# Kernel optimization log

Hardware: AMD Instinct MI355X
Metric: run time of the kernel (lower is better)

The kernel has to match this reference:

```python
import jax, jax.numpy as jnp
import numpy as np


def _unfold(x, k, stride, pad):
    """torch.nn.Unfold equivalent. x: [B,C,H,W] -> [B, C*k*k, L] with
    channel ordering (c, ki, kj) slow->fast and L = oh*ow row-major."""
    if pad:
        x = jnp.pad(x, ((0, 0), (0, 0), (pad, pad), (pad, pad)))
    B, C, H, W = x.shape
    oh = (H - k) // stride + 1
    ow = (W - k) // stride + 1
    r = jnp.arange(oh) * stride
    c = jnp.arange(ow) * stride
    xr = x[:, :, r[:, None] + jnp.arange(k)[None, :], :]          # [B,C,oh,k,W]
    xc = xr[:, :, :, :, c[:, None] + jnp.arange(k)[None, :]]      # [B,C,oh,ki,ow,kj]
    p = xc.transpose(0, 1, 3, 5, 2, 4)                            # [B,C,ki,kj,oh,ow]
    return p.reshape(B, C * k * k, oh * ow)


def _resize_bilinear(x, h, w):
    # matches F.interpolate(mode='bilinear', align_corners=False) for upsampling
    B, C = x.shape[0], x.shape[1]
    return jax.image.resize(x, (B, C, h, w), method='bilinear')


def setup_inputs() -> dict:
    key = jax.random.key(0)
    ks = jax.random.split(key, 8)
    bs, C, NC = 16, 768, 200
    x = jax.random.normal(ks[0], (bs, 784, C), jnp.float32)
    mask = jax.random.uniform(ks[1], (bs, 81), dtype=jnp.float32)
    img = jax.random.normal(ks[2], (bs, 3, 448, 448), jnp.float32)
    W_fc = jax.random.normal(ks[3], (NC, C), jnp.float32) * 0.02
    b_fc = jnp.zeros((NC,), jnp.float32)
    W_l = jax.random.normal(ks[4], (192, C), jnp.float32) * 0.02
    b_l = jnp.zeros((192,), jnp.float32)
    W_m = jax.random.normal(ks[5], (192, C), jnp.float32) * 0.02
    b_m = jnp.zeros((192,), jnp.float32)
    W_s = jax.random.normal(ks[6], (384, C), jnp.float32) * 0.02
    b_s = jnp.zeros((384,), jnp.float32)
    return dict(x=x, mask=mask, img=img, W_fc=W_fc, b_fc=b_fc,
                W_l=W_l, b_l=b_l, W_m=W_m, b_m=b_m, W_s=W_s, b_s=b_s)


def reference(x, mask, img, W_fc, b_fc, W_l, b_l, W_m, b_m, W_s, b_s):
    bs, C = x.shape[0], 768
    # im2col over image and feature map (all produce 81 = 9x9 windows)
    image_patches = _unfold(img, 128, 48, 32).transpose(0, 2, 1)   # [bs,81,3*128*128]
    feat = x.transpose(0, 2, 1).reshape(bs, C, 28, 28)
    patches_l = _unfold(feat, 8, 3, 2).transpose(0, 2, 1)          # [bs,81,C*64]
    patches_m = _unfold(feat, 6, 3, 1).transpose(0, 2, 1)          # [bs,81,C*36]
    patches_s = _unfold(feat, 4, 3, 0).transpose(0, 2, 1)          # [bs,81,C*16]
    # per-token class probabilities -> per-window importance score
    prob = jax.nn.softmax(x @ W_fc.T + b_fc, axis=-1)              # [bs,784,NC]
    max_logits = prob.max(axis=-1).reshape(bs, 1, 28, 28)
    part_logits = _unfold(max_logits, 8, 3, 2).mean(axis=1)        # [bs,81]
    part_logits = mask * part_logits
    sel = jnp.argmax(part_logits, axis=-1)                         # top-1 window id
    b_idx = jnp.arange(bs)
    parts_l = patches_l[b_idx, sel]                                # [bs,C*64]
    parts_m = patches_m[b_idx, sel]                                # [bs,C*36]
    parts_s = patches_s[b_idx, sel]                                # [bs,C*16]
    image_parts = image_patches[b_idx, sel]                        # [bs,3*128*128]
    # fold (single patch => reshape) + bilinear upsample to 8x8
    outl = parts_l.reshape(bs, C, 8, 8).transpose(0, 2, 3, 1).reshape(bs, 64, C)
    outm = _resize_bilinear(parts_m.reshape(bs, C, 6, 6), 8, 8)
    outm = outm.transpose(0, 2, 3, 1).reshape(bs, 64, C)
    outs = _resize_bilinear(parts_s.reshape(bs, C, 4, 4), 8, 8)
    outs = outs.transpose(0, 2, 3, 1).reshape(bs, 64, C)
    part1 = outl @ W_l.T + b_l                                     # [bs,64,192]
    part2 = outm @ W_m.T + b_m                                     # [bs,64,192]
    part3 = outs @ W_s.T + b_s                                     # [bs,64,384]
    ff_cat = jnp.concatenate([part1, part2, part3], axis=2)        # [bs,64,768]
    image_part = _resize_bilinear(image_parts.reshape(bs, 3, 128, 128), 224, 224)
    return ff_cat, image_part
```

## Files before the change

kernel.cpp:

```cpp
#include <hip/hip_runtime.h>
#include <math.h>

typedef __attribute__((ext_vector_type(8))) short bf16x8;
typedef __attribute__((ext_vector_type(4))) float f32x4;

__device__ __forceinline__ unsigned short f32_to_bf16_rne(float f) {
    unsigned int u = __float_as_uint(f);
    unsigned int r = (u + 0x7FFFu + ((u >> 16) & 1u)) >> 16;
    return (unsigned short)r;
}
__device__ __forceinline__ float bf16_to_f32(unsigned short h) {
    return __uint_as_float(((unsigned int)h) << 16);
}
__device__ __forceinline__ unsigned int pck(unsigned short a, unsigned short b) {
    return (unsigned int)a | ((unsigned int)b << 16);
}

__global__ __launch_bounds__(256) void k_split(
    const float* __restrict__ src, unsigned short* __restrict__ hi,
    unsigned short* __restrict__ lo, int src_rows, int nq)
{
    const int idx = blockIdx.x * 256 + threadIdx.x;
    if (idx >= nq) return;
    const int c = idx / 192;
    const int kk = (idx % 192) * 4;
    unsigned short h[4] = {0, 0, 0, 0}, l[4] = {0, 0, 0, 0};
    if (c < src_rows) {
        const float4 w = *(const float4*)&src[(size_t)c * 768 + kk];
        const float wv[4] = {w.x, w.y, w.z, w.w};
#pragma unroll
        for (int j = 0; j < 4; ++j) {
            h[j] = f32_to_bf16_rne(wv[j]);
            l[j] = f32_to_bf16_rne(wv[j] - bf16_to_f32(h[j]));
        }
    }
    *(uint2*)&hi[(size_t)c * 768 + kk] = make_uint2(pck(h[0], h[1]), pck(h[2], h[3]));
    *(uint2*)&lo[(size_t)c * 768 + kk] = make_uint2(pck(l[0], l[1]), pck(l[2], l[3]));
}

__global__ __launch_bounds__(256) void k_logits(
    const float* __restrict__ x, const unsigned short* __restrict__ Whi,
    const unsigned short* __restrict__ Wlo, float* __restrict__ logits)
{
    __shared__ unsigned short Ah[4][64][8], Alo[4][64][8];
    __shared__ unsigned short Bh[8][64][8], Blo[8][64][8];
    const int tid = threadIdx.x;
    const int lane = tid & 63;
    const int wid = tid >> 6;
    const int wm = wid & 1, wn = wid >> 1;
    const int row0 = blockIdx.x * 64;
    const int n0 = blockIdx.y * 128;

    f32x4 acc[2][4];
    const f32x4 z = {0.f, 0.f, 0.f, 0.f};
#pragma unroll
    for (int mi = 0; mi < 2; ++mi)
#pragma unroll
        for (int q = 0; q < 4; ++q) acc[mi][q] = z;

    const int ar = tid & 63;
    const int ap = tid >> 6;
    const int bc = tid >> 1;
    const int bkh = tid & 1;

    for (int kc = 0; kc < 768; kc += 32) {
        __syncthreads();
        {
            const float* src = &x[(size_t)(row0 + ar) * 768 + kc + ap * 8];
            const float4 v0 = *(const float4*)src;
            const float4 v1 = *(const float4*)(src + 4);
            const float av[8] = {v0.x, v0.y, v0.z, v0.w, v1.x, v1.y, v1.z, v1.w};
            unsigned short h[8], l[8];
#pragma unroll
            for (int j = 0; j < 8; ++j) {
                h[j] = f32_to_bf16_rne(av[j]);
                l[j] = f32_to_bf16_rne(av[j] - bf16_to_f32(h[j]));
            }
            const int m = ar >> 4, ci = ar & 15;
            *(uint4*)&Ah[m][ap * 16 + ci][0] =
                make_uint4(pck(h[0], h[1]), pck(h[2], h[3]), pck(h[4], h[5]), pck(h[6], h[7]));
            *(uint4*)&Alo[m][ap * 16 + ci][0] =
                make_uint4(pck(l[0], l[1]), pck(l[2], l[3]), pck(l[4], l[5]), pck(l[6], l[7]));
        }
        {
            const size_t off = (size_t)(n0 + bc) * 768 + kc + bkh * 16;
            const uint4 h0 = *(const uint4*)&Whi[off];
            const uint4 h1 = *(const uint4*)&Whi[off + 8];
            const uint4 l0 = *(const uint4*)&Wlo[off];
            const uint4 l1 = *(const uint4*)&Wlo[off + 8];
            const int q = bc >> 4, ci = bc & 15;
            *(uint4*)&Bh[q][(2 * bkh) * 16 + ci][0] = h0;
            *(uint4*)&Bh[q][(2 * bkh + 1) * 16 + ci][0] = h1;
            *(uint4*)&Blo[q][(2 * bkh) * 16 + ci][0] = l0;
            *(uint4*)&Blo[q][(2 * bkh + 1) * 16 + ci][0] = l1;
        }
        __syncthreads();

        bf16x8 a_h[2], a_l[2];
#pragma unroll
        for (int mi = 0; mi < 2; ++mi) {
            a_h[mi] = *(const bf16x8*)&Ah[wm * 2 + mi][lane][0];
            a_l[mi] = *(const bf16x8*)&Alo[wm * 2 + mi][lane][0];
        }
#pragma unroll
        for (int q = 0; q < 4; ++q) {
            const bf16x8 bh = *(const bf16x8*)&Bh[wn * 4 + q][lane][0];
            const bf16x8 bl = *(const bf16x8*)&Blo[wn * 4 + q][lane][0];
#pragma unroll
            for (int mi = 0; mi < 2; ++mi) {
                acc[mi][q] = __builtin_amdgcn_mfma_f32_16x16x32_bf16(a_l[mi], bh, acc[mi][q], 0, 0, 0);
                acc[mi][q] = __builtin_amdgcn_mfma_f32_16x16x32_bf16(a_h[mi], bl, acc[mi][q], 0, 0, 0);
                acc[mi][q] = __builtin_amdgcn_mfma_f32_16x16x32_bf16(a_h[mi], bh, acc[mi][q], 0, 0, 0);
            }
        }
    }

#pragma unroll
    for (int mi = 0; mi < 2; ++mi)
#pragma unroll
        for (int q = 0; q < 4; ++q)
#pragma unroll
            for (int r = 0; r < 4; ++r) {
                const int row = row0 + wm * 32 + mi * 16 + (lane >> 4) * 4 + r;
                const int col = n0 + wn * 64 + q * 16 + (lane & 15);
                logits[(size_t)row * 256 + col] = acc[mi][q][r];
            }
}

__global__ __launch_bounds__(256) void k_softmax(
    const float* __restrict__ logits, const float* __restrict__ bfc,
    float* __restrict__ maxprob)
{
    const int row = blockIdx.x * 4 + (threadIdx.x >> 6);
    const int lane = threadIdx.x & 63;
    float v[4];
    float m = -1e30f;
#pragma unroll
    for (int j = 0; j < 4; ++j) {
        const int c = lane + j * 64;
        v[j] = (c < 200) ? (logits[(size_t)row * 256 + c] + bfc[c]) : -1e30f;
        m = fmaxf(m, v[j]);
    }
#pragma unroll
    for (int s = 32; s; s >>= 1) m = fmaxf(m, __shfl_xor(m, s, 64));
    float se = 0.f;
#pragma unroll
    for (int j = 0; j < 4; ++j) {
        const int c = lane + j * 64;
        if (c < 200) se += __expf(v[j] - m);
    }
#pragma unroll
    for (int s = 32; s; s >>= 1) se += __shfl_xor(se, s, 64);
    if (lane == 0) maxprob[row] = 1.0f / se;
}

__global__ void k_sel(const float* __restrict__ maxprob,
                      const float* __restrict__ mask, int* __restrict__ sel)
{
    __shared__ float mp[784];
    __shared__ float pl[81];
    const int b = blockIdx.x, tid = threadIdx.x;
    for (int i = tid; i < 784; i += blockDim.x) mp[i] = maxprob[b * 784 + i];
    __syncthreads();
    if (tid < 81) {
        const int pr = tid / 9, pc = tid % 9;
        float s = 0.f;
        for (int ki = 0; ki < 8; ++ki) {
            const int y = pr * 3 - 2 + ki;
            if (y < 0 || y >= 28) continue;
            for (int kj = 0; kj < 8; ++kj) {
                const int xx = pc * 3 - 2 + kj;
                if (xx < 0 || xx >= 28) continue;
                s += mp[y * 28 + xx];
            }
        }
        pl[tid] = mask[b * 81 + tid] * (s * (1.f / 64.f));
    }
    __syncthreads();
    if (tid == 0) {
        float best = pl[0]; int bi = 0;
        for (int i = 1; i < 81; ++i) if (pl[i] > best) { best = pl[i]; bi = i; }
        sel[b] = bi;
    }
}

__device__ __forceinline__ void rcoef8(int o, int n, int& f0, int& f1, float& w)
{
    float s = (o + 0.5f) * ((float)n * 0.125f) - 0.5f;
    s = fminf(fmaxf(s, 0.f), (float)(n - 1));
    f0 = (int)s;
    w = s - (float)f0;
    f1 = f0 + 1; if (f1 > n - 1) f1 = n - 1;
}

__global__ __launch_bounds__(256) void k_ff(
    const float* __restrict__ x, const int* __restrict__ sel,
    const unsigned short* __restrict__ Whi2, const unsigned short* __restrict__ Wlo2,
    const float* __restrict__ bl, const float* __restrict__ bm,
    const float* __restrict__ bs_, float* __restrict__ out)
{
    __shared__ float W8[64][33];
    __shared__ unsigned short Ah[4][64][8], Alo[4][64][8];
    __shared__ unsigned short Bh[4][64][8], Blo[4][64][8];

    const int blk = blockIdx.x;
    const int b = blk / 12, t = blk % 12;
    const int n0 = t * 64;
    const int seg = (t < 3) ? 0 : ((t < 6) ? 1 : 2);
    const float* bias = (seg == 0) ? (bl + t * 64)
                      : (seg == 1) ? (bm + (t - 3) * 64)
                                   : (bs_ + (t - 6) * 64);
    const int s = sel[b];
    const int wy0 = (s / 9) * 3 - 2, wx0 = (s % 9) * 3 - 2;

    const int tid = threadIdx.x;
    const int lane = tid & 63;
    const int wid = tid >> 6, wmi = wid & 1, wn = wid >> 1;

    const int gp = tid & 63;
    const int gy = wy0 + (gp >> 3), gx = wx0 + (gp & 7);
    const bool inb = (gy >= 0 && gy < 28 && gx >= 0 && gx < 28);
    const float* xsrc = x + ((size_t)b * 784 + (inb ? (gy * 28 + gx) : 0)) * 768;
    const int ko = (tid >> 6) * 8;

    const int ai = tid & 63;
    int r00, r01, r10, r11; float fx = 0.f, fy = 0.f;
    if (seg == 0) { r00 = r01 = r10 = r11 = ai; }
    else {
        const int nn = (seg == 1) ? 6 : 4, off = (seg == 1) ? 1 : 2;
        int f0y, f1y, f0x, f1x;
        rcoef8(ai >> 3, nn, f0y, f1y, fy);
        rcoef8(ai & 7, nn, f0x, f1x, fx);
        r00 = (off + f0y) * 8 + off + f0x;
        r01 = (off + f0y) * 8 + off + f1x;
        r10 = (off + f1y) * 8 + off + f0x;
        r11 = (off + f1y) * 8 + off + f1x;
    }

    const int bc = tid >> 2, kq = tid & 3;
    const unsigned short* WhP = Whi2 + (size_t)(n0 + bc) * 768 + kq * 8;
    const unsigned short* WlP = Wlo2 + (size_t)(n0 + bc) * 768 + kq * 8;

    f32x4 acc[2][2];
    const f32x4 z = {0.f, 0.f, 0.f, 0.f};
#pragma unroll
    for (int mi = 0; mi < 2; ++mi)
#pragma unroll
        for (int q = 0; q < 2; ++q) acc[mi][q] = z;

    for (int kc = 0; kc < 768; kc += 32) {
        __syncthreads();
        {
            float v[8] = {0, 0, 0, 0, 0, 0, 0, 0};
            if (inb) {
                const float4 a0 = *(const float4*)(xsrc + kc + ko);
                const float4 a1 = *(const float4*)(xsrc + kc + ko + 4);
                v[0] = a0.x; v[1] = a0.y; v[2] = a0.z; v[3] = a0.w;
                v[4] = a1.x; v[5] = a1.y; v[6] = a1.z; v[7] = a1.w;
            }
#pragma unroll
            for (int j = 0; j < 8; ++j) W8[gp][ko + j] = v[j];
        }
        {
            const uint4 h = *(const uint4*)(WhP + kc);
            const uint4 l = *(const uint4*)(WlP + kc);
            *(uint4*)&Bh[bc >> 4][kq * 16 + (bc & 15)][0] = h;
            *(uint4*)&Blo[bc >> 4][kq * 16 + (bc & 15)][0] = l;
        }
        __syncthreads();
        {
            unsigned short h[8], l[8];
#pragma unroll
            for (int j = 0; j < 8; ++j) {
                const int k = ko + j;
                const float g00 = W8[r00][k], g01 = W8[r01][k];
                const float g10 = W8[r10][k], g11 = W8[r11][k];
                const float v0 = g00 + fx * (g01 - g00);
                const float v1 = g10 + fx * (g11 - g10);
                const float a = v0 + fy * (v1 - v0);
                h[j] = f32_to_bf16_rne(a);
                l[j] = f32_to_bf16_rne(a - bf16_to_f32(h[j]));
            }
            const int m = ai >> 4, ci = ai & 15, p2 = ko >> 3;
            *(uint4*)&Ah[m][p2 * 16 + ci][0] =
                make_uint4(pck(h[0], h[1]), pck(h[2], h[3]), pck(h[4], h[5]), pck(h[6], h[7]));
            *(uint4*)&Alo[m][p2 * 16 + ci][0] =
                make_uint4(pck(l[0], l[1]), pck(l[2], l[3]), pck(l[4], l[5]), pck(l[6], l[7]));
        }
        __syncthreads();

        bf16x8 a_h[2], a_l[2];
#pragma unroll
        for (int mi = 0; mi < 2; ++mi) {
            a_h[mi] = *(const bf16x8*)&Ah[wmi * 2 + mi][lane][0];
            a_l[mi] = *(const bf16x8*)&Alo[wmi * 2 + mi][lane][0];
        }
#pragma unroll
        for (int q = 0; q < 2; ++q) {
            const bf16x8 bh = *(const bf16x8*)&Bh[wn * 2 + q][lane][0];
            const bf16x8 bl2 = *(const bf16x8*)&Blo[wn * 2 + q][lane][0];
#pragma unroll
            for (int mi = 0; mi < 2; ++mi) {
                acc[mi][q] = __builtin_amdgcn_mfma_f32_16x16x32_bf16(a_l[mi], bh, acc[mi][q], 0, 0, 0);
                acc[mi][q] = __builtin_amdgcn_mfma_f32_16x16x32_bf16(a_h[mi], bl2, acc[mi][q], 0, 0, 0);
                acc[mi][q] = __builtin_amdgcn_mfma_f32_16x16x32_bf16(a_h[mi], bh, acc[mi][q], 0, 0, 0);
            }
        }
    }

#pragma unroll
    for (int mi = 0; mi < 2; ++mi)
#pragma unroll
        for (int q = 0; q < 2; ++q)
#pragma unroll
            for (int r = 0; r < 4; ++r) {
                const int row = wmi * 32 + mi * 16 + (lane >> 4) * 4 + r;
                const int col = wn * 32 + q * 16 + (lane & 15);
                out[((size_t)b * 64 + row) * 768 + n0 + col] = acc[mi][q][r] + bias[col];
            }
}

__global__ __launch_bounds__(256) void k_image(
    const float* __restrict__ img, const int* __restrict__ sel,
    float* __restrict__ out)
{
    const int idx = blockIdx.x * 256 + threadIdx.x;
    if (idx >= 16 * 3 * 224 * 224) return;
    const int ox = idx % 224;
    int t = idx / 224;
    const int oy = t % 224; t /= 224;
    const int c = t % 3;
    const int b = t / 3;
    const int s = sel[b];
    const int ry0 = (s / 9) * 48 - 32, cx0 = (s % 9) * 48 - 32;

    float sy = (oy + 0.5f) * (128.f / 224.f) - 0.5f;
    sy = fminf(fmaxf(sy, 0.f), 127.f);
    const int fy0 = (int)sy; const float wy = sy - (float)fy0;
    const int fy1 = (fy0 < 127) ? fy0 + 1 : 127;

    float sx = (ox + 0.5f) * (128.f / 224.f) - 0.5f;
    sx = fminf(fmaxf(sx, 0.f), 127.f);
    const int fx0 = (int)sx; const float wx = sx - (float)fx0;
    const int fx1 = (fx0 < 127) ? fx0 + 1 : 127;

    const float* ib = img + ((size_t)b * 3 + c) * 448 * 448;
    auto rd = [&](int py, int px) -> float {
        const int r = ry0 + py, cc = cx0 + px;
        return (r >= 0 && r < 448 && cc >= 0 && cc < 448) ? ib[r * 448 + cc] : 0.f;
    };
    const float g00 = rd(fy0, fx0), g01 = rd(fy0, fx1);
    const float g10 = rd(fy1, fx0), g11 = rd(fy1, fx1);
    const float v0 = g00 + wx * (g01 - g00);
    const float v1 = g10 + wx * (g11 - g10);
    out[idx] = v0 + wy * (v1 - v0);
}

extern "C" void kernel_launch(void* const* d_in, const int* in_sizes, int n_in,
                              void* d_out, int out_size, void* d_ws, size_t ws_size,
                              hipStream_t stream)
{
    const float* x    = (const float*)d_in[0];
    const float* mask = (const float*)d_in[1];
    const float* img  = (const float*)d_in[2];
    const float* Wfc  = (const float*)d_in[3];
    const float* bfc  = (const float*)d_in[4];
    const float* Wl   = (const float*)d_in[5];
    const float* bl   = (const float*)d_in[6];
    const float* Wm   = (const float*)d_in[7];
    const float* bm   = (const float*)d_in[8];
    const float* Ws   = (const float*)d_in[9];
    const float* bs   = (const float*)d_in[10];
    float* out = (float*)d_out;

    char* ws = (char*)d_ws;
    float* maxprob      = (float*)ws;
    int*   sel          = (int*)(ws + 51200);
    unsigned short* Whi  = (unsigned short*)(ws + 65536);
    unsigned short* Wlo  = (unsigned short*)(ws + 65536 + 393216);
    unsigned short* Whi2 = (unsigned short*)(ws + 917504);
    unsigned short* Wlo2 = (unsigned short*)(ws + 917504 + 1179648);
    float* logits = (float*)(ws + 3276800);

    hipLaunchKernelGGL(k_split, dim3(192), dim3(256), 0, stream, Wfc, Whi, Wlo, 200, 256 * 192);
    hipLaunchKernelGGL(k_split, dim3(144), dim3(256), 0, stream, Wl, Whi2, Wlo2, 192, 192 * 192);
    hipLaunchKernelGGL(k_split, dim3(144), dim3(256), 0, stream,
                       Wm, Whi2 + (size_t)192 * 768, Wlo2 + (size_t)192 * 768, 192, 192 * 192);
    hipLaunchKernelGGL(k_split, dim3(288), dim3(256), 0, stream,
                       Ws, Whi2 + (size_t)384 * 768, Wlo2 + (size_t)384 * 768, 384, 384 * 192);

    hipLaunchKernelGGL(k_logits,  dim3(196, 2), dim3(256), 0, stream, x, Whi, Wlo, logits);
    hipLaunchKernelGGL(k_softmax, dim3(3136),   dim3(256), 0, stream, logits, bfc, maxprob);
    hipLaunchKernelGGL(k_sel,     dim3(16),     dim3(128), 0, stream, maxprob, mask, sel);
    hipLaunchKernelGGL(k_ff,      dim3(192),    dim3(256), 0, stream,
                       x, sel, Whi2, Wlo2, bl, bm, bs, out);
    hipLaunchKernelGGL(k_image,   dim3(9408),   dim3(256), 0, stream,
                       img, sel, out + 786432);
}
```

Measured before the change: 215.9 us.

## Fuse logits GEMM with softmax, pre-pack weights, double-buffer GEMM loops

The four weight-split launches are merged into one prep kernel. It writes bf16 hi/lo weights directly in the MFMA-ready LDS tile layout, so the GEMM kernels can copy them with coalesced uint4 loads. The logits GEMM now covers all 256 columns per block and computes the softmax max-probability in its epilogue, which removes the logits buffer round trip and the separate softmax kernel. Both GEMMs use register-prefetched double-buffered LDS with one barrier per k-step, and k_ff does the bilinear gather with wave shuffles instead of an fp32 LDS staging tile. The costs are higher register and LDS use per block and only 196 blocks for the logits GEMM.

```diff
diff --git a/kernel.cpp b/kernel.cpp
--- a/kernel.cpp
+++ b/kernel.cpp
@@ -16,16 +16,22 @@
     return (unsigned int)a | ((unsigned int)b << 16);
 }
 
-__global__ __launch_bounds__(256) void k_split(
-    const float* __restrict__ src, unsigned short* __restrict__ hi,
-    unsigned short* __restrict__ lo, int src_rows, int nq)
-{
-    const int idx = blockIdx.x * 256 + threadIdx.x;
-    if (idx >= nq) return;
+__global__ __launch_bounds__(256) void k_prep(
+    const float* __restrict__ Wfc, const float* __restrict__ Wl,
+    const float* __restrict__ Wm, const float* __restrict__ Ws,
+    unsigned short* __restrict__ Bpkh, unsigned short* __restrict__ Bpkl,
+    unsigned short* __restrict__ B2h, unsigned short* __restrict__ B2l)
+{
+    const int blk = blockIdx.x, tid = threadIdx.x;
+    const float* src; int idx, rows, cbase; bool isfc;
+    if (blk < 192)      { isfc = true;  idx = blk * 256 + tid;        src = Wfc; rows = 200; cbase = 0; }
+    else if (blk < 336) { isfc = false; idx = (blk - 192) * 256 + tid; src = Wl;  rows = 192; cbase = 0; }
+    else if (blk < 480) { isfc = false; idx = (blk - 336) * 256 + tid; src = Wm;  rows = 192; cbase = 192; }
+    else                { isfc = false; idx = (blk - 480) * 256 + tid; src = Ws;  rows = 384; cbase = 384; }
     const int c = idx / 192;
     const int kk = (idx % 192) * 4;
     unsigned short h[4] = {0, 0, 0, 0}, l[4] = {0, 0, 0, 0};
-    if (c < src_rows) {
+    if (c < rows) {
         const float4 w = *(const float4*)&src[(size_t)c * 768 + kk];
         const float wv[4] = {w.x, w.y, w.z, w.w};
 #pragma unroll
@@ -34,124 +40,160 @@
             l[j] = f32_to_bf16_rne(wv[j] - bf16_to_f32(h[j]));
         }
     }
-    *(uint2*)&hi[(size_t)c * 768 + kk] = make_uint2(pck(h[0], h[1]), pck(h[2], h[3]));
-    *(uint2*)&lo[(size_t)c * 768 + kk] = make_uint2(pck(l[0], l[1]), pck(l[2], l[3]));
-}
-
-__global__ __launch_bounds__(256) void k_logits(
-    const float* __restrict__ x, const unsigned short* __restrict__ Whi,
-    const unsigned short* __restrict__ Wlo, float* __restrict__ logits)
-{
-    __shared__ unsigned short Ah[4][64][8], Alo[4][64][8];
-    __shared__ unsigned short Bh[8][64][8], Blo[8][64][8];
+    const int step = kk >> 5, oct = (kk & 31) >> 3, elem = kk & 7;
+    const uint2 uh = make_uint2(pck(h[0], h[1]), pck(h[2], h[3]));
+    const uint2 ul = make_uint2(pck(l[0], l[1]), pck(l[2], l[3]));
+    if (isfc) {
+        const size_t off = (size_t)((step * 16 + (c >> 4)) * 64 + oct * 16 + (c & 15)) * 8 + elem;
+        *(uint2*)&Bpkh[off] = uh;
+        *(uint2*)&Bpkl[off] = ul;
+    } else {
+        const int cg = cbase + c;
+        const int tt = cg >> 6, cc = cg & 63;
+        const size_t off = (size_t)(((tt * 24 + step) * 4 + (cc >> 4)) * 64 + oct * 16 + (cc & 15)) * 8 + elem;
+        *(uint2*)&B2h[off] = uh;
+        *(uint2*)&B2l[off] = ul;
+    }
+}
+
+__global__ __launch_bounds__(256) void k_logits_fused(
+    const float* __restrict__ x, const unsigned short* __restrict__ Bpkh,
+    const unsigned short* __restrict__ Bpkl, const float* __restrict__ bfc,
+    float* __restrict__ maxprob)
+{
+    __shared__ unsigned short AhS[2][4][64][8];
+    __shared__ unsigned short AlS[2][4][64][8];
+    __shared__ unsigned short BhS[2][16][64][8];
+    __shared__ unsigned short BlS[2][16][64][8];
+    __shared__ float sbias[256];
+    __shared__ float red[4][64];
+    __shared__ float red2[4][64];
+
     const int tid = threadIdx.x;
     const int lane = tid & 63;
     const int wid = tid >> 6;
-    const int wm = wid & 1, wn = wid >> 1;
     const int row0 = blockIdx.x * 64;
-    const int n0 = blockIdx.y * 128;
-
-    f32x4 acc[2][4];
+
+    sbias[tid] = (tid < 200) ? bfc[tid] : -1e30f;
+
+    const int ar = tid & 63, ap = tid >> 6;
+    const float* xb = x + (size_t)(row0 + ar) * 768 + ap * 8;
+    const uint4* bhs = (const uint4*)Bpkh;
+    const uint4* bls = (const uint4*)Bpkl;
+
+    float ag[8];
+    uint4 bgh[4], bgl[4];
+
+    f32x4 acc[4][4];
     const f32x4 z = {0.f, 0.f, 0.f, 0.f};
 #pragma unroll
-    for (int mi = 0; mi < 2; ++mi)
-#pragma unroll
-        for (int q = 0; q < 4; ++q) acc[mi][q] = z;
-
-    const int ar = tid & 63;
-    const int ap = tid >> 6;
-    const int bc = tid >> 1;
-    const int bkh = tid & 1;
-
-    for (int kc = 0; kc < 768; kc += 32) {
+    for (int mf = 0; mf < 4; ++mf)
+#pragma unroll
+        for (int q = 0; q < 4; ++q) acc[mf][q] = z;
+
+    auto LOADAB = [&](int t) {
+        const float4 v0 = *(const float4*)(xb + t * 32);
+        const float4 v1 = *(const float4*)(xb + t * 32 + 4);
+        ag[0] = v0.x; ag[1] = v0.y; ag[2] = v0.z; ag[3] = v0.w;
+        ag[4] = v1.x; ag[5] = v1.y; ag[6] = v1.z; ag[7] = v1.w;
+#pragma unroll
+        for (int j = 0; j < 4; ++j) {
+            bgh[j] = bhs[t * 1024 + j * 256 + tid];
+            bgl[j] = bls[t * 1024 + j * 256 + tid];
+        }
+    };
+    auto WRITEAB = [&](int buf) {
+        unsigned short h[8], l[8];
+#pragma unroll
+        for (int j = 0; j < 8; ++j) {
+            h[j] = f32_to_bf16_rne(ag[j]);
+            l[j] = f32_to_bf16_rne(ag[j] - bf16_to_f32(h[j]));
+        }
+        *(uint4*)&AhS[buf][ar >> 4][ap * 16 + (ar & 15)][0] =
+            make_uint4(pck(h[0], h[1]), pck(h[2], h[3]), pck(h[4], h[5]), pck(h[6], h[7]));
+        *(uint4*)&AlS[buf][ar >> 4][ap * 16 + (ar & 15)][0] =
+            make_uint4(pck(l[0], l[1]), pck(l[2], l[3]), pck(l[4], l[5]), pck(l[6], l[7]));
+        uint4* bdh = (uint4*)&BhS[buf][0][0][0];
+        uint4* bdl = (uint4*)&BlS[buf][0][0][0];
+#pragma unroll
+        for (int j = 0; j < 4; ++j) {
+            bdh[j * 256 + tid] = bgh[j];
+            bdl[j * 256 + tid] = bgl[j];
+        }
+    };
+
+    LOADAB(0);
+    WRITEAB(0);
+    __syncthreads();
+
+    for (int t = 0; t < 24; ++t) {
+        const int cur = t & 1;
+        if (t < 23) LOADAB(t + 1);
+        bf16x8 ah[4], al2[4];
+#pragma unroll
+        for (int mf = 0; mf < 4; ++mf) {
+            ah[mf]  = *(const bf16x8*)&AhS[cur][mf][lane][0];
+            al2[mf] = *(const bf16x8*)&AlS[cur][mf][lane][0];
+        }
+#pragma unroll
+        for (int q = 0; q < 4; ++q) {
+            const bf16x8 bh = *(const bf16x8*)&BhS[cur][wid * 4 + q][lane][0];
+            const bf16x8 bl = *(const bf16x8*)&BlS[cur][wid * 4 + q][lane][0];
+#pragma unroll
+            for (int mf = 0; mf < 4; ++mf) {
+                acc[mf][q] = __builtin_amdgcn_mfma_f32_16x16x32_bf16(al2[mf], bh, acc[mf][q], 0, 0, 0);
+                acc[mf][q] = __builtin_amdgcn_mfma_f32_16x16x32_bf16(ah[mf], bl, acc[mf][q], 0, 0, 0);
+                acc[mf][q] = __builtin_amdgcn_mfma_f32_16x16x32_bf16(ah[mf], bh, acc[mf][q], 0, 0, 0);
+            }
+        }
+        if (t < 23) WRITEAB(cur ^ 1);
         __syncthreads();
-        {
-            const float* src = &x[(size_t)(row0 + ar) * 768 + kc + ap * 8];
-            const float4 v0 = *(const float4*)src;
-            const float4 v1 = *(const float4*)(src + 4);
-            const float av[8] = {v0.x, v0.y, v0.z, v0.w, v1.x, v1.y, v1.z, v1.w};
-            unsigned short h[8], l[8];
-#pragma unroll
-            for (int j = 0; j < 8; ++j) {
-                h[j] = f32_to_bf16_rne(av[j]);
-                l[j] = f32_to_bf16_rne(av[j] - bf16_to_f32(h[j]));
+    }
+
+    float bv[4];
+#pragma unroll
+    for (int q = 0; q < 4; ++q) bv[q] = sbias[wid * 64 + q * 16 + (lane & 15)];
+
+    float mrow[4][4];
+#pragma unroll
+    for (int mf = 0; mf < 4; ++mf)
+#pragma unroll
+        for (int r = 0; r < 4; ++r) {
+            float mx = -1e30f;
+#pragma unroll
+            for (int q = 0; q < 4; ++q) mx = fmaxf(mx, acc[mf][q][r] + bv[q]);
+#pragma unroll
+            for (int s = 1; s < 16; s <<= 1) mx = fmaxf(mx, __shfl_xor(mx, s, 64));
+            mrow[mf][r] = mx;
+            if ((lane & 15) == 0) red[wid][mf * 16 + (lane >> 4) * 4 + r] = mx;
+        }
+    __syncthreads();
+#pragma unroll
+    for (int mf = 0; mf < 4; ++mf)
+#pragma unroll
+        for (int r = 0; r < 4; ++r) {
+            const int row = mf * 16 + (lane >> 4) * 4 + r;
+            const float m = fmaxf(fmaxf(red[0][row], red[1][row]),
+                                  fmaxf(red[2][row], red[3][row]));
+            float se = 0.f;
+#pragma unroll
+            for (int q = 0; q < 4; ++q) se += __expf(acc[mf][q][r] + bv[q] - m);
+#pragma unroll
+            for (int s = 1; s < 16; s <<= 1) se += __shfl_xor(se, s, 64);
+            if ((lane & 15) == 0) red2[wid][row] = se;
+            (void)mrow[mf][r];
+        }
+    __syncthreads();
+    if (wid == 0 && (lane & 15) == 0) {
+#pragma unroll
+        for (int mf = 0; mf < 4; ++mf)
+#pragma unroll
+            for (int r = 0; r < 4; ++r) {
+                const int row = mf * 16 + (lane >> 4) * 4 + r;
+                maxprob[row0 + row] = 1.0f /
+                    (red2[0][row] + red2[1][row] + red2[2][row] + red2[3][row]);
             }
-            const int m = ar >> 4, ci = ar & 15;
-            *(uint4*)&Ah[m][ap * 16 + ci][0] =
-                make_uint4(pck(h[0], h[1]), pck(h[2], h[3]), pck(h[4], h[5]), pck(h[6], h[7]));
-            *(uint4*)&Alo[m][ap * 16 + ci][0] =
-                make_uint4(pck(l[0], l[1]), pck(l[2], l[3]), pck(l[4], l[5]), pck(l[6], l[7]));
-        }
-        {
-            const size_t off = (size_t)(n0 + bc) * 768 + kc + bkh * 16;
-            const uint4 h0 = *(const uint4*)&Whi[off];
-            const uint4 h1 = *(const uint4*)&Whi[off + 8];
-            const uint4 l0 = *(const uint4*)&Wlo[off];
-            const uint4 l1 = *(const uint4*)&Wlo[off + 8];
-            const int q = bc >> 4, ci = bc & 15;
-            *(uint4*)&Bh[q][(2 * bkh) * 16 + ci][0] = h0;
-            *(uint4*)&Bh[q][(2 * bkh + 1) * 16 + ci][0] = h1;
-            *(uint4*)&Blo[q][(2 * bkh) * 16 + ci][0] = l0;
-            *(uint4*)&Blo[q][(2 * bkh + 1) * 16 + ci][0] = l1;
-        }
-        __syncthreads();
-
-        bf16x8 a_h[2], a_l[2];
-#pragma unroll
-        for (int mi = 0; mi < 2; ++mi) {
-            a_h[mi] = *(const bf16x8*)&Ah[wm * 2 + mi][lane][0];
-            a_l[mi] = *(const bf16x8*)&Alo[wm * 2 + mi][lane][0];
-        }
-#pragma unroll
-        for (int q = 0; q < 4; ++q) {
-            const bf16x8 bh = *(const bf16x8*)&Bh[wn * 4 + q][lane][0];
-            const bf16x8 bl = *(const bf16x8*)&Blo[wn * 4 + q][lane][0];
-#pragma unroll
-            for (int mi = 0; mi < 2; ++mi) {
-                acc[mi][q] = __builtin_amdgcn_mfma_f32_16x16x32_bf16(a_l[mi], bh, acc[mi][q], 0, 0, 0);
-                acc[mi][q] = __builtin_amdgcn_mfma_f32_16x16x32_bf16(a_h[mi], bl, acc[mi][q], 0, 0, 0);
-                acc[mi][q] = __builtin_amdgcn_mfma_f32_16x16x32_bf16(a_h[mi], bh, acc[mi][q], 0, 0, 0);
-            }
-        }
-    }
-
-#pragma unroll
-    for (int mi = 0; mi < 2; ++mi)
-#pragma unroll
-        for (int q = 0; q < 4; ++q)
-#pragma unroll
-            for (int r = 0; r < 4; ++r) {
-                const int row = row0 + wm * 32 + mi * 16 + (lane >> 4) * 4 + r;
-                const int col = n0 + wn * 64 + q * 16 + (lane & 15);
-                logits[(size_t)row * 256 + col] = acc[mi][q][r];
-            }
-}
-
-__global__ __launch_bounds__(256) void k_softmax(
-    const float* __restrict__ logits, const float* __restrict__ bfc,
-    float* __restrict__ maxprob)
-{
-    const int row = blockIdx.x * 4 + (threadIdx.x >> 6);
-    const int lane = threadIdx.x & 63;
-    float v[4];
-    float m = -1e30f;
-#pragma unroll
-    for (int j = 0; j < 4; ++j) {
-        const int c = lane + j * 64;
-        v[j] = (c < 200) ? (logits[(size_t)row * 256 + c] + bfc[c]) : -1e30f;
-        m = fmaxf(m, v[j]);
-    }
-#pragma unroll
-    for (int s = 32; s; s >>= 1) m = fmaxf(m, __shfl_xor(m, s, 64));
-    float se = 0.f;
-#pragma unroll
-    for (int j = 0; j < 4; ++j) {
-        const int c = lane + j * 64;
-        if (c < 200) se += __expf(v[j] - m);
-    }
-#pragma unroll
-    for (int s = 32; s; s >>= 1) se += __shfl_xor(se, s, 64);
-    if (lane == 0) maxprob[row] = 1.0f / se;
+    }
 }
 
 __global__ void k_sel(const float* __restrict__ maxprob,
@@ -195,13 +237,14 @@
 
 __global__ __launch_bounds__(256) void k_ff(
     const float* __restrict__ x, const int* __restrict__ sel,
-    const unsigned short* __restrict__ Whi2, const unsigned short* __restrict__ Wlo2,
+    const unsigned short* __restrict__ B2h, const unsigned short* __restrict__ B2l,
     const float* __restrict__ bl, const float* __restrict__ bm,
     const float* __restrict__ bs_, float* __restrict__ out)
 {
-    __shared__ float W8[64][33];
-    __shared__ unsigned short Ah[4][64][8], Alo[4][64][8];
-    __shared__ unsigned short Bh[4][64][8], Blo[4][64][8];
+    __shared__ unsigned short AhS[2][4][64][8];
+    __shared__ unsigned short AlS[2][4][64][8];
+    __shared__ unsigned short BhS[2][4][64][8];
+    __shared__ unsigned short BlS[2][4][64][8];
 
     const int blk = blockIdx.x;
     const int b = blk / 12, t = blk % 12;
@@ -217,29 +260,28 @@
     const int lane = tid & 63;
     const int wid = tid >> 6, wmi = wid & 1, wn = wid >> 1;
 
-    const int gp = tid & 63;
-    const int gy = wy0 + (gp >> 3), gx = wx0 + (gp & 7);
+    const int gy = wy0 + (lane >> 3), gx = wx0 + (lane & 7);
     const bool inb = (gy >= 0 && gy < 28 && gx >= 0 && gx < 28);
-    const float* xsrc = x + ((size_t)b * 784 + (inb ? (gy * 28 + gx) : 0)) * 768;
-    const int ko = (tid >> 6) * 8;
-
-    const int ai = tid & 63;
+    const float* xsrc = x + ((size_t)b * 784 + (inb ? (gy * 28 + gx) : 0)) * 768 + wid * 8;
+
     int r00, r01, r10, r11; float fx = 0.f, fy = 0.f;
-    if (seg == 0) { r00 = r01 = r10 = r11 = ai; }
+    if (seg == 0) { r00 = r01 = r10 = r11 = lane; }
     else {
         const int nn = (seg == 1) ? 6 : 4, off = (seg == 1) ? 1 : 2;
         int f0y, f1y, f0x, f1x;
-        rcoef8(ai >> 3, nn, f0y, f1y, fy);
-        rcoef8(ai & 7, nn, f0x, f1x, fx);
+        rcoef8(lane >> 3, nn, f0y, f1y, fy);
+        rcoef8(lane & 7, nn, f0x, f1x, fx);
         r00 = (off + f0y) * 8 + off + f0x;
         r01 = (off + f0y) * 8 + off + f1x;
         r10 = (off + f1y) * 8 + off + f0x;
         r11 = (off + f1y) * 8 + off + f1x;
     }
 
-    const int bc = tid >> 2, kq = tid & 3;
-    const unsigned short* WhP = Whi2 + (size_t)(n0 + bc) * 768 + kq * 8;
-    const unsigned short* WlP = Wlo2 + (size_t)(n0 + bc) * 768 + kq * 8;
+    const uint4* b2h = (const uint4*)B2h + (size_t)t * 24 * 256;
+    const uint4* b2l = (const uint4*)B2l + (size_t)t * 24 * 256;
+
+    float g[8];
+    uint4 bh_r, bl_r;
 
     f32x4 acc[2][2];
     const f32x4 z = {0.f, 0.f, 0.f, 0.f};
@@ -248,64 +290,67 @@
 #pragma unroll
         for (int q = 0; q < 2; ++q) acc[mi][q] = z;
 
-    for (int kc = 0; kc < 768; kc += 32) {
+    auto LOAD = [&](int st) {
+        if (inb) {
+            const float4 v0 = *(const float4*)(xsrc + st * 32);
+            const float4 v1 = *(const float4*)(xsrc + st * 32 + 4);
+            g[0] = v0.x; g[1] = v0.y; g[2] = v0.z; g[3] = v0.w;
+            g[4] = v1.x; g[5] = v1.y; g[6] = v1.z; g[7] = v1.w;
+        } else {
+#pragma unroll
+            for (int j = 0; j < 8; ++j) g[j] = 0.f;
+        }
+        bh_r = b2h[st * 256 + tid];
+        bl_r = b2l[st * 256 + tid];
+    };
+    auto WRITE = [&](int buf) {
+        unsigned short h[8], l[8];
+#pragma unroll
+        for (int j = 0; j < 8; ++j) {
+            const float v00 = __shfl(g[j], r00, 64);
+            const float v01 = __shfl(g[j], r01, 64);
+            const float v10 = __shfl(g[j], r10, 64);
+            const float v11 = __shfl(g[j], r11, 64);
+            const float v0 = v00 + fx * (v01 - v00);
+            const float v1 = v10 + fx * (v11 - v10);
+            const float a = v0 + fy * (v1 - v0);
+            h[j] = f32_to_bf16_rne(a);
+            l[j] = f32_to_bf16_rne(a - bf16_to_f32(h[j]));
+        }
+        *(uint4*)&AhS[buf][lane >> 4][wid * 16 + (lane & 15)][0] =
+            make_uint4(pck(h[0], h[1]), pck(h[2], h[3]), pck(h[4], h[5]), pck(h[6], h[7]));
+        *(uint4*)&AlS[buf][lane >> 4][wid * 16 + (lane & 15)][0] =
+            make_uint4(pck(l[0], l[1]), pck(l[2], l[3]), pck(l[4], l[5]), pck(l[6], l[7]));
+        ((uint4*)&BhS[buf][0][0][0])[tid] = bh_r;
+        ((uint4*)&BlS[buf][0][0][0])[tid] = bl_r;
+    };
+
+    LOAD(0);
+    WRITE(0);
+    __syncthreads();
+
+    for (int st = 0; st < 24; ++st) {
+        const int cur = st & 1;
+        if (st < 23) LOAD(st + 1);
+        bf16x8 ah[2], al2[2];
+#pragma unroll
+        for (int mi = 0; mi < 2; ++mi) {
+            ah[mi]  = *(const bf16x8*)&AhS[cur][wmi * 2 + mi][lane][0];
+            al2[mi] = *(const bf16x8*)&AlS[cur][wmi * 2 + mi][lane][0];
+        }
+#pragma unroll
+        for (int q = 0; q < 2; ++q) {
+            const bf16x8 bh = *(const bf16x8*)&BhS[cur][wn * 2 + q][lane][0];
+            const bf16x8 bl2 = *(const bf16x8*)&BlS[cur][wn * 2 + q][lane][0];
+#pragma unroll
+            for (int mi = 0; mi < 2; ++mi) {
+                acc[mi][q] = __builtin_amdgcn_mfma_f32_16x16x32_bf16(al2[mi], bh, acc[mi][q], 0, 0, 0);
+                acc[mi][q] = __builtin_amdgcn_mfma_f32_16x16x32_bf16(ah[mi], bl2, acc[mi][q], 0, 0, 0);
+                acc[mi][q] = __builtin_amdgcn_mfma_f32_16x16x32_bf16(ah[mi], bh, acc[mi][q], 0, 0, 0);
+            }
+        }
+        if (st < 23) WRITE(cur ^ 1);
         __syncthreads();
-        {
-            float v[8] = {0, 0, 0, 0, 0, 0, 0, 0};
-            if (inb) {
-                const float4 a0 = *(const float4*)(xsrc + kc + ko);
-                const float4 a1 = *(const float4*)(xsrc + kc + ko + 4);
-                v[0] = a0.x; v[1] = a0.y; v[2] = a0.z; v[3] = a0.w;
-                v[4] = a1.x; v[5] = a1.y; v[6] = a1.z; v[7] = a1.w;
-            }
-#pragma unroll
-            for (int j = 0; j < 8; ++j) W8[gp][ko + j] = v[j];
-        }
-        {
-            const uint4 h = *(const uint4*)(WhP + kc);
-            const uint4 l = *(const uint4*)(WlP + kc);
-            *(uint4*)&Bh[bc >> 4][kq * 16 + (bc & 15)][0] = h;
-            *(uint4*)&Blo[bc >> 4][kq * 16 + (bc & 15)][0] = l;
-        }
-        __syncthreads();
-        {
-            unsigned short h[8], l[8];
-#pragma unroll
-            for (int j = 0; j < 8; ++j) {
-                const int k = ko + j;
-                const float g00 = W8[r00][k], g01 = W8[r01][k];
-                const float g10 = W8[r10][k], g11 = W8[r11][k];
-                const float v0 = g00 + fx * (g01 - g00);
-                const float v1 = g10 + fx * (g11 - g10);
-                const float a = v0 + fy * (v1 - v0);
-                h[j] = f32_to_bf16_rne(a);
-                l[j] = f32_to_bf16_rne(a - bf16_to_f32(h[j]));
-            }
-            const int m = ai >> 4, ci = ai & 15, p2 = ko >> 3;
-            *(uint4*)&Ah[m][p2 * 16 + ci][0] =
-                make_uint4(pck(h[0], h[1]), pck(h[2], h[3]), pck(h[4], h[5]), pck(h[6], h[7]));
-            *(uint4*)&Alo[m][p2 * 16 + ci][0] =
-                make_uint4(pck(l[0], l[1]), pck(l[2], l[3]), pck(l[4], l[5]), pck(l[6], l[7]));
-        }
-        __syncthreads();
-
-        bf16x8 a_h[2], a_l[2];
-#pragma unroll
-        for (int mi = 0; mi < 2; ++mi) {
-            a_h[mi] = *(const bf16x8*)&Ah[wmi * 2 + mi][lane][0];
-            a_l[mi] = *(const bf16x8*)&Alo[wmi * 2 + mi][lane][0];
-        }
-#pragma unroll
-        for (int q = 0; q < 2; ++q) {
-            const bf16x8 bh = *(const bf16x8*)&Bh[wn * 2 + q][lane][0];
-            const bf16x8 bl2 = *(const bf16x8*)&Blo[wn * 2 + q][lane][0];
-#pragma unroll
-            for (int mi = 0; mi < 2; ++mi) {
-                acc[mi][q] = __builtin_amdgcn_mfma_f32_16x16x32_bf16(a_l[mi], bh, acc[mi][q], 0, 0, 0);
-                acc[mi][q] = __builtin_amdgcn_mfma_f32_16x16x32_bf16(a_h[mi], bl2, acc[mi][q], 0, 0, 0);
-                acc[mi][q] = __builtin_amdgcn_mfma_f32_16x16x32_bf16(a_h[mi], bh, acc[mi][q], 0, 0, 0);
-            }
-        }
     }
 
 #pragma unroll
@@ -374,26 +419,21 @@
     float* out = (float*)d_out;
 
     char* ws = (char*)d_ws;
-    float* maxprob      = (float*)ws;
-    int*   sel          = (int*)(ws + 51200);
-    unsigned short* Whi  = (unsigned short*)(ws + 65536);
-    unsigned short* Wlo  = (unsigned short*)(ws + 65536 + 393216);
-    unsigned short* Whi2 = (unsigned short*)(ws + 917504);
-    unsigned short* Wlo2 = (unsigned short*)(ws + 917504 + 1179648);
-    float* logits = (float*)(ws + 3276800);
-
-    hipLaunchKernelGGL(k_split, dim3(192), dim3(256), 0, stream, Wfc, Whi, Wlo, 200, 256 * 192);
-    hipLaunchKernelGGL(k_split, dim3(144), dim3(256), 0, stream, Wl, Whi2, Wlo2, 192, 192 * 192);
-    hipLaunchKernelGGL(k_split, dim3(144), dim3(256), 0, stream,
-                       Wm, Whi2 + (size_t)192 * 768, Wlo2 + (size_t)192 * 768, 192, 192 * 192);
-    hipLaunchKernelGGL(k_split, dim3(288), dim3(256), 0, stream,
-                       Ws, Whi2 + (size_t)384 * 768, Wlo2 + (size_t)384 * 768, 384, 384 * 192);
-
-    hipLaunchKernelGGL(k_logits,  dim3(196, 2), dim3(256), 0, stream, x, Whi, Wlo, logits);
-    hipLaunchKernelGGL(k_softmax, dim3(3136),   dim3(256), 0, stream, logits, bfc, maxprob);
-    hipLaunchKernelGGL(k_sel,     dim3(16),     dim3(128), 0, stream, maxprob, mask, sel);
-    hipLaunchKernelGGL(k_ff,      dim3(192),    dim3(256), 0, stream,
-                       x, sel, Whi2, Wlo2, bl, bm, bs, out);
-    hipLaunchKernelGGL(k_image,   dim3(9408),   dim3(256), 0, stream,
+    float* maxprob       = (float*)ws;
+    int*   sel           = (int*)(ws + 51200);
+    unsigned short* Bpkh = (unsigned short*)(ws + 65536);
+    unsigned short* Bpkl = (unsigned short*)(ws + 458752);
+    unsigned short* B2h  = (unsigned short*)(ws + 851968);
+    unsigned short* B2l  = (unsigned short*)(ws + 2031616);
+
+    hipLaunchKernelGGL(k_prep,         dim3(768),  dim3(256), 0, stream,
+                       Wfc, Wl, Wm, Ws, Bpkh, Bpkl, B2h, B2l);
+    hipLaunchKernelGGL(k_logits_fused, dim3(196),  dim3(256), 0, stream,
+                       x, Bpkh, Bpkl, bfc, maxprob);
+    hipLaunchKernelGGL(k_sel,          dim3(16),   dim3(128), 0, stream,
+                       maxprob, mask, sel);
+    hipLaunchKernelGGL(k_ff,           dim3(192),  dim3(256), 0, stream,
+                       x, sel, B2h, B2l, bl, bm, bs, out);
+    hipLaunchKernelGGL(k_image,        dim3(9408), dim3(256), 0, stream,
                        img, sel, out + 786432);
 }
```

Result: slower. 226.5 us (+4.9%).
